# Kernel optimization log

Hardware: AMD Instinct MI355X
Metric: run time of the kernel (lower is better)

Reference implementation:

```python
import jax, jax.numpy as jnp
import numpy as np

N_NODES = 50000
N_EDGES = 800000
D = 128


def sage_conv(x, src, dst, w_nbr, w_root, b, n_nodes):
    # mean aggregation of neighbor features: messages flow src (j) -> dst (i)
    msg_sum = jax.ops.segment_sum(x[src], dst, num_segments=n_nodes)  # [N, D]
    deg = jax.ops.segment_sum(jnp.ones((src.shape[0],), x.dtype), dst,
                              num_segments=n_nodes)
    mean = msg_sum / jnp.maximum(deg, 1.0)[:, None]
    # PyG SAGEConv: lin_l(aggr) + lin_r(x); bias lives in lin_l
    return mean @ w_nbr + x @ w_root + b


def setup_inputs() -> dict:
    key = jax.random.key(0)
    ks = jax.random.split(key, 16)
    s = 1.0 / np.sqrt(D)
    inp = {
        "x": jax.random.normal(ks[0], (N_NODES, D), jnp.float32),
        "edge_index": jax.random.randint(ks[1], (2, N_EDGES), 0, N_NODES,
                                         dtype=jnp.int64),
    }
    for l in range(3):
        inp[f"w_nbr{l}"] = jax.random.normal(ks[2 + 3 * l], (D, D), jnp.float32) * s
        inp[f"w_root{l}"] = jax.random.normal(ks[3 + 3 * l], (D, D), jnp.float32) * s
        inp[f"b{l}"] = jnp.zeros((D,), jnp.float32)
    inp["w_cls"] = jax.random.normal(ks[12], (D, 1), jnp.float32) * s
    inp["b_cls"] = jnp.zeros((1,), jnp.float32)
    return inp


def reference(x, edge_index, w_nbr0, w_root0, b0, w_nbr1, w_root1, b1,
              w_nbr2, w_root2, b2, w_cls, b_cls):
    src, dst = edge_index[0], edge_index[1]
    n = x.shape[0]
    layers = [(w_nbr0, w_root0, b0), (w_nbr1, w_root1, b1), (w_nbr2, w_root2, b2)]
    h = x
    for i, (wn, wr, b) in enumerate(layers):
        h = sage_conv(h, src, dst, wn, wr, b, n)
        if i < len(layers) - 1:
            h = jax.nn.relu(h)  # dropout is identity in eval mode
    return (h @ w_cls + b_cls).squeeze(-1)  # [N]
```

## Files before the change

### kernel.cpp

```cpp
#include <hip/hip_runtime.h>

#define N_NODES 50000
#define N_EDGES 800000
#define D 128
#define NGROUPS 3125
#define NE4 200000
#define NB_E4 782

typedef __attribute__((ext_vector_type(8))) short short8;
typedef __attribute__((ext_vector_type(4))) float f32x4;

__device__ __forceinline__ float bits2f(unsigned int u) {
    union { unsigned int u; float f; } c; c.u = u; return c.f;
}
__device__ __forceinline__ unsigned short f2b(float f) {
    union { float f; unsigned int u; } c; c.f = f;
    unsigned int r = c.u + 0x7fffu + ((c.u >> 16) & 1u);
    return (unsigned short)(r >> 16);
}


__global__ void k_big(const int* __restrict__ dst, int* __restrict__ deg,
                      int* __restrict__ rank, const float* __restrict__ x,
                      const float* __restrict__ wn0, const float* __restrict__ wr0,
                      const float* __restrict__ wn1, const float* __restrict__ wr1,
                      const float* __restrict__ wn2, const float* __restrict__ wr2,
                      const float* __restrict__ b2, const float* __restrict__ wc,
                      const float* __restrict__ bc,
                      unsigned short* __restrict__ f0,
                      unsigned short* __restrict__ f1,
                      unsigned short* __restrict__ f2,
                      unsigned short* __restrict__ Bp,
                      float* __restrict__ uvc) {
    int b = blockIdx.x;
    if (b < NB_E4) {
        int i = b * 256 + threadIdx.x;
        if (i < NE4) {
            int4 d4 = reinterpret_cast<const int4*>(dst)[i];
            int r0 = atomicAdd(&deg[d4.x], 1);
            int r1 = atomicAdd(&deg[d4.y], 1);
            int r2 = atomicAdd(&deg[d4.z], 1);
            int r3 = atomicAdd(&deg[d4.w], 1);
            reinterpret_cast<int4*>(rank)[i] = make_int4(r0, r1, r2, r3);
        }
    } else if (b < 7032) {
        int i = (b - NB_E4) * 256 + threadIdx.x;
        float4 v = reinterpret_cast<const float4*>(x)[i];
        ushort4 o;
        o.x = f2b(v.x); o.y = f2b(v.y); o.z = f2b(v.z); o.w = f2b(v.w);
        reinterpret_cast<ushort4*>(f0)[i] = o;
    } else if (b < 7064) {
        int t = (b - 7032) * 256 + threadIdx.x;
        int layer = t >> 12;
        int rem = t & 4095;
        int kstep = rem >> 9;
        int cf = (rem >> 6) & 7;
        int lane = t & 63;
        const float* W = (kstep < 4) ? (layer ? wn1 : wn0) : (layer ? wr1 : wr0);
        int kb = kstep * 32 + (lane >> 4) * 8;
        int colv = cf * 16 + (lane & 15);
        int koff = (kstep < 4) ? kb : kb - 128;
        unsigned short* dstp = Bp + (((layer * 64 + kstep * 8 + cf) * 64 + lane) << 3);
        #pragma unroll
        for (int i = 0; i < 8; ++i) dstp[i] = f2b(W[(koff + i) * D + colv]);
    } else if (b == 7064) {
        int t = threadIdx.x;
        if (t < D) {
            f0[(size_t)N_NODES * D + t] = 0;
            f1[(size_t)N_NODES * D + t] = 0;
            f2[(size_t)N_NODES * D + t] = 0;
        }
    } else {
        int t = threadIdx.x;
        if (t < 128) {
            float su = 0.f;
            for (int m = 0; m < 128; ++m) su += wn2[t * D + m] * wc[m];
            uvc[t] = su;
        } else {
            int k = t - 128;
            float sv = 0.f;
            for (int m = 0; m < 128; ++m) sv += wr2[k * D + m] * wc[m];
            uvc[128 + k] = sv;
        }
        if (t == 0) {
            float sc = 0.f;
            for (int m = 0; m < 128; ++m) sc += b2[m] * wc[m];
            uvc[256] = sc + bc[0];
        }
    }
}


__global__ void k_scan1(const int* __restrict__ deg, int* __restrict__ rs,
                        int* __restrict__ bsum) {
    __shared__ int wsum[16];
    int tid = threadIdx.x;
    int lane = tid & 63, wid = tid >> 6;
    int i = blockIdx.x * 1024 + tid;
    int v = (i < N_NODES) ? deg[i] : 0;
    int s = v;
    #pragma unroll
    for (int off = 1; off < 64; off <<= 1) {
        int t = __shfl_up(s, off, 64);
        if (lane >= off) s += t;
    }
    if (lane == 63) wsum[wid] = s;
    __syncthreads();
    if (tid < 64) {
        int wv = (tid < 16) ? wsum[tid] : 0;
        int t = wv;
        #pragma unroll
        for (int off = 1; off < 16; off <<= 1) {
            int u = __shfl_up(t, off, 64);
            if (tid >= off) t += u;
        }
        if (tid < 16) wsum[tid] = t - wv;
    }
    __syncthreads();
    int excl = s - v + wsum[wid];
    if (i < N_NODES) rs[i] = excl;
    if (tid == 1023) bsum[blockIdx.x] = excl + v;
}

__global__ void k_scan23(int* __restrict__ rs, const int* __restrict__ bsum,
                         int nb) {
    __shared__ int bp[64];
    if (threadIdx.x < 64) {
        int lane = threadIdx.x;
        int v = (lane < nb) ? bsum[lane] : 0;
        int s = v;
        #pragma unroll
        for (int off = 1; off < 64; off <<= 1) {
            int t = __shfl_up(s, off, 64);
            if (lane >= off) s += t;
        }
        bp[lane] = s - v;
    }
    __syncthreads();
    int i = blockIdx.x * blockDim.x + threadIdx.x;
    if (i < N_NODES) rs[i] += bp[i >> 10];
    if (i == 0) rs[N_NODES] = N_EDGES;
}

__global__ void k_fill2(const int* __restrict__ src, const int* __restrict__ dst,
                        const int* __restrict__ rs, const int* __restrict__ rank,
                        int* __restrict__ col) {
    int i = blockIdx.x * blockDim.x + threadIdx.x;
    if (i >= NE4) return;
    int4 d4 = reinterpret_cast<const int4*>(dst)[i];
    int4 r4 = reinterpret_cast<const int4*>(rank)[i];
    int4 s4 = reinterpret_cast<const int4*>(src)[i];
    int p0 = rs[d4.x], p1 = rs[d4.y], p2 = rs[d4.z], p3 = rs[d4.w];
    col[p0 + r4.x] = s4.x;
    col[p1 + r4.y] = s4.y;
    col[p2 + r4.z] = s4.z;
    col[p3 + r4.w] = s4.w;
}


#define ACCUM(v)                                                      \
    acc0 += bits2f((v).x << 16); acc1 += bits2f((v).x & 0xffff0000u); \
    acc2 += bits2f((v).y << 16); acc3 += bits2f((v).y & 0xffff0000u); \
    acc4 += bits2f((v).z << 16); acc5 += bits2f((v).z & 0xffff0000u); \
    acc6 += bits2f((v).w << 16); acc7 += bits2f((v).w & 0xffff0000u);

__global__ __launch_bounds__(256) void k_agg2(const unsigned short* __restrict__ h,
                                              const int* __restrict__ rs,
                                              const int* __restrict__ col,
                                              unsigned short* __restrict__ mean) {
    const int lane = threadIdx.x & 63;
    const int node = blockIdx.x * 4 + (threadIdx.x >> 6);
    if (node >= N_NODES) return;
    const int j0 = rs[node], j1 = rs[node + 1];
    const int deg = j1 - j0;
    const int q = lane >> 4;
    const int d8 = (lane & 15) * 8;

    int myc = (j0 + lane < j1) ? col[j0 + lane] : N_NODES;
    const int nfull = deg < 64 ? deg : 64;
    const int nb = (nfull + 15) >> 4;

    float acc0 = 0.f, acc1 = 0.f, acc2 = 0.f, acc3 = 0.f;
    float acc4 = 0.f, acc5 = 0.f, acc6 = 0.f, acc7 = 0.f;

    for (int i = 0; i < nb; ++i) {
        int t = (i << 4) + q;
        int c0 = __shfl(myc, t, 64);
        int c1 = __shfl(myc, t + 4, 64);
        int c2 = __shfl(myc, t + 8, 64);
        int c3 = __shfl(myc, t + 12, 64);
        uint4 v0 = *(const uint4*)(h + (size_t)c0 * D + d8);
        uint4 v1 = *(const uint4*)(h + (size_t)c1 * D + d8);
        uint4 v2 = *(const uint4*)(h + (size_t)c2 * D + d8);
        uint4 v3 = *(const uint4*)(h + (size_t)c3 * D + d8);
        ACCUM(v0); ACCUM(v1); ACCUM(v2); ACCUM(v3);
    }
    for (int j = j0 + 64 + q; j < j1; j += 4) {
        int c = col[j];
        uint4 v = *(const uint4*)(h + (size_t)c * D + d8);
        ACCUM(v);
    }

    acc0 += __shfl_xor(acc0, 16, 64); acc0 += __shfl_xor(acc0, 32, 64);
    acc1 += __shfl_xor(acc1, 16, 64); acc1 += __shfl_xor(acc1, 32, 64);
    acc2 += __shfl_xor(acc2, 16, 64); acc2 += __shfl_xor(acc2, 32, 64);
    acc3 += __shfl_xor(acc3, 16, 64); acc3 += __shfl_xor(acc3, 32, 64);
    acc4 += __shfl_xor(acc4, 16, 64); acc4 += __shfl_xor(acc4, 32, 64);
    acc5 += __shfl_xor(acc5, 16, 64); acc5 += __shfl_xor(acc5, 32, 64);
    acc6 += __shfl_xor(acc6, 16, 64); acc6 += __shfl_xor(acc6, 32, 64);
    acc7 += __shfl_xor(acc7, 16, 64); acc7 += __shfl_xor(acc7, 32, 64);

    if (lane < 16) {
        float s = 1.0f / (float)(deg > 0 ? deg : 1);
        uint4 o;
        o.x = (unsigned int)f2b(acc0 * s) | ((unsigned int)f2b(acc1 * s) << 16);
        o.y = (unsigned int)f2b(acc2 * s) | ((unsigned int)f2b(acc3 * s) << 16);
        o.z = (unsigned int)f2b(acc4 * s) | ((unsigned int)f2b(acc5 * s) << 16);
        o.w = (unsigned int)f2b(acc6 * s) | ((unsigned int)f2b(acc7 * s) << 16);
        *reinterpret_cast<uint4*>(mean + (size_t)node * D + d8) = o;
    }
}


__global__ __launch_bounds__(256) void k_gemm(
    const unsigned short* __restrict__ Amean, const unsigned short* __restrict__ Ah,
    const unsigned short* __restrict__ Bp, const float* __restrict__ bias,
    unsigned short* __restrict__ outh) {
    int lane = threadIdx.x & 63;
    int w = blockIdx.x * 4 + (threadIdx.x >> 6);
    int g0 = w * 2;
    if (g0 >= NGROUPS) return;
    int g1ok = (g0 + 1 < NGROUPS);
    int hl = lane & 15;
    int klane = (lane >> 4) * 8;
    int arow0 = g0 * 16 + hl;
    int arow1 = g0 * 16 + 16 + hl;
    if (arow1 > N_NODES) arow1 = N_NODES;

    f32x4 acc0[8], acc1[8];
    #pragma unroll
    for (int i = 0; i < 8; ++i) { acc0[i] = (f32x4)0.0f; acc1[i] = (f32x4)0.0f; }

    const short8* bpv = reinterpret_cast<const short8*>(Bp);
    #pragma unroll
    for (int kstep = 0; kstep < 8; ++kstep) {
        const unsigned short* Asrc = (kstep < 4) ? Amean : Ah;
        int kk = (kstep & 3) * 32 + klane;
        short8 a0 = *reinterpret_cast<const short8*>(Asrc + (size_t)arow0 * D + kk);
        short8 a1 = *reinterpret_cast<const short8*>(Asrc + (size_t)arow1 * D + kk);
        #pragma unroll
        for (int cf = 0; cf < 8; ++cf) {
            short8 b = bpv[(kstep * 8 + cf) * 64 + lane];
            acc0[cf] = __builtin_amdgcn_mfma_f32_16x16x32_bf16(a0, b, acc0[cf], 0, 0, 0);
            acc1[cf] = __builtin_amdgcn_mfma_f32_16x16x32_bf16(a1, b, acc1[cf], 0, 0, 0);
        }
    }

    int rbase0 = g0 * 16 + (lane >> 4) * 4;
    #pragma unroll
    for (int cf = 0; cf < 8; ++cf) {
        int bcol = cf * 16 + hl;
        float bv = bias[bcol];
        #pragma unroll
        for (int i = 0; i < 4; ++i) {
            float v = fmaxf(acc0[cf][i] + bv, 0.f);
            outh[(size_t)(rbase0 + i) * D + bcol] = f2b(v);
            if (g1ok) {
                float v1 = fmaxf(acc1[cf][i] + bv, 0.f);
                outh[(size_t)(rbase0 + 16 + i) * D + bcol] = f2b(v1);
            }
        }
    }
}


__global__ __launch_bounds__(256) void k_gemm_dot(
    const unsigned short* __restrict__ Amean, const unsigned short* __restrict__ Ah,
    const unsigned short* __restrict__ Bp, const float* __restrict__ bias,
    const float* __restrict__ uvc, float* __restrict__ s, float* __restrict__ t) {
    int lane = threadIdx.x & 63;
    int w = blockIdx.x * 4 + (threadIdx.x >> 6);
    int g0 = w * 2;
    if (g0 >= NGROUPS) return;
    int g1ok = (g0 + 1 < NGROUPS);
    int hl = lane & 15;
    int klane = (lane >> 4) * 8;
    int arow0 = g0 * 16 + hl;
    int arow1 = g0 * 16 + 16 + hl;
    if (arow1 > N_NODES) arow1 = N_NODES;

    f32x4 acc0[8], acc1[8];
    #pragma unroll
    for (int i = 0; i < 8; ++i) { acc0[i] = (f32x4)0.0f; acc1[i] = (f32x4)0.0f; }

    const short8* bpv = reinterpret_cast<const short8*>(Bp);
    #pragma unroll
    for (int kstep = 0; kstep < 8; ++kstep) {
        const unsigned short* Asrc = (kstep < 4) ? Amean : Ah;
        int kk = (kstep & 3) * 32 + klane;
        short8 a0 = *reinterpret_cast<const short8*>(Asrc + (size_t)arow0 * D + kk);
        short8 a1 = *reinterpret_cast<const short8*>(Asrc + (size_t)arow1 * D + kk);
        #pragma unroll
        for (int cf = 0; cf < 8; ++cf) {
            short8 b = bpv[(kstep * 8 + cf) * 64 + lane];
            acc0[cf] = __builtin_amdgcn_mfma_f32_16x16x32_bf16(a0, b, acc0[cf], 0, 0, 0);
            acc1[cf] = __builtin_amdgcn_mfma_f32_16x16x32_bf16(a1, b, acc1[cf], 0, 0, 0);
        }
    }

    float ps0[4] = {0.f, 0.f, 0.f, 0.f}, pt0[4] = {0.f, 0.f, 0.f, 0.f};
    float ps1[4] = {0.f, 0.f, 0.f, 0.f}, pt1[4] = {0.f, 0.f, 0.f, 0.f};
    #pragma unroll
    for (int cf = 0; cf < 8; ++cf) {
        int bcol = cf * 16 + hl;
        float bv = bias[bcol];
        float uu = uvc[bcol];
        float vv = uvc[128 + bcol];
        #pragma unroll
        for (int i = 0; i < 4; ++i) {
            float v = fmaxf(acc0[cf][i] + bv, 0.f);
            ps0[i] += v * uu;
            pt0[i] += v * vv;
            float v1 = fmaxf(acc1[cf][i] + bv, 0.f);
            ps1[i] += v1 * uu;
            pt1[i] += v1 * vv;
        }
    }
    #pragma unroll
    for (int m = 1; m < 16; m <<= 1) {
        #pragma unroll
        for (int i = 0; i < 4; ++i) {
            ps0[i] += __shfl_xor(ps0[i], m, 64);
            pt0[i] += __shfl_xor(pt0[i], m, 64);
            ps1[i] += __shfl_xor(ps1[i], m, 64);
            pt1[i] += __shfl_xor(pt1[i], m, 64);
        }
    }
    if (hl == 0) {
        int rbase0 = g0 * 16 + (lane >> 4) * 4;
        #pragma unroll
        for (int i = 0; i < 4; ++i) {
            s[rbase0 + i] = ps0[i];
            t[rbase0 + i] = pt0[i];
            if (g1ok) {
                s[rbase0 + 16 + i] = ps1[i];
                t[rbase0 + 16 + i] = pt1[i];
            }
        }
    }
}

__global__ __launch_bounds__(256) void k_sagg2(const float* __restrict__ s,
                                               const float* __restrict__ t,
                                               const float* __restrict__ uvc,
                                               const int* __restrict__ rs,
                                               const int* __restrict__ col,
                                               float* __restrict__ out) {
    const int lane = threadIdx.x & 63;
    const int hl = lane & 15;
    const int node = blockIdx.x * 16 + (threadIdx.x >> 6) * 4 + (lane >> 4);
    const int j0 = rs[node], j1 = rs[node + 1];
    float sm = 0.f;
    for (int j = j0 + hl; j < j1; j += 16) sm += s[col[j]];
    #pragma unroll
    for (int m = 1; m < 16; m <<= 1) sm += __shfl_xor(sm, m, 64);
    if (hl == 0) {
        int deg = j1 - j0;
        out[node] = sm / (float)(deg > 0 ? deg : 1) + t[node] + uvc[256];
    }
}


extern "C" void kernel_launch(void* const* d_in, const int* in_sizes, int n_in,
                              void* d_out, int out_size, void* d_ws,
                              size_t ws_size, hipStream_t stream) {
    const float* x = (const float*)d_in[0];
    const int* ei = (const int*)d_in[1];
    const int* src = ei;
    const int* dst = ei + N_EDGES;
    const float* wn[3] = {(const float*)d_in[2], (const float*)d_in[5],
                          (const float*)d_in[8]};
    const float* wr[3] = {(const float*)d_in[3], (const float*)d_in[6],
                          (const float*)d_in[9]};
    const float* bs[3] = {(const float*)d_in[4], (const float*)d_in[7],
                          (const float*)d_in[10]};
    const float* wc = (const float*)d_in[11];
    const float* bc = (const float*)d_in[12];
    float* out = (float*)d_out;

    char* ws = (char*)d_ws;
    size_t off = 0;
    auto alloc = [&](size_t bytes) -> void* {
        void* p = (void*)(ws + off);
        off += (bytes + 255) & ~(size_t)255;
        return p;
    };
    const size_t frows = (size_t)(N_NODES + 1) * D;
    int* deg = (int*)alloc(N_NODES * 4);
    int* rs = (int*)alloc((N_NODES + 1) * 4);
    int* rank = (int*)alloc(N_EDGES * 4);
    int* bsum = (int*)alloc(64 * 4);
    int* col = (int*)alloc(N_EDGES * 4);
    unsigned short* f0 = (unsigned short*)alloc(frows * 2);
    unsigned short* f1 = (unsigned short*)alloc(frows * 2);
    unsigned short* f2 = (unsigned short*)alloc(frows * 2);
    unsigned short* Bp = (unsigned short*)alloc(2 * 256 * 128 * 2);
    float* uvc = (float*)alloc(260 * 4);
    float* sbuf = (float*)alloc(N_NODES * 4);
    float* tbuf = (float*)alloc(N_NODES * 4);

    hipMemsetAsync(deg, 0, N_NODES * 4, stream);

    k_big<<<7066, 256, 0, stream>>>(dst, deg, rank, x, wn[0], wr[0], wn[1],
                                    wr[1], wn[2], wr[2], bs[2], wc, bc,
                                    f0, f1, f2, Bp, uvc);

    int nb = (N_NODES + 1023) / 1024;
    k_scan1<<<nb, 1024, 0, stream>>>(deg, rs, bsum);
    k_scan23<<<(N_NODES + 255) / 256, 256, 0, stream>>>(rs, bsum, nb);
    k_fill2<<<NB_E4, 256, 0, stream>>>(src, dst, rs, rank, col);

    const int agg_grid = (N_NODES + 3) / 4;
    const int gemm_grid = ((NGROUPS + 1) / 2 + 3) / 4;
    unsigned short* Bp0 = Bp;
    unsigned short* Bp1 = Bp + 256 * 128;

    k_agg2<<<agg_grid, 256, 0, stream>>>(f0, rs, col, f1);
    k_gemm<<<gemm_grid, 256, 0, stream>>>(f1, f0, Bp0, bs[0], f2);
    k_agg2<<<agg_grid, 256, 0, stream>>>(f2, rs, col, f0);
    k_gemm_dot<<<gemm_grid, 256, 0, stream>>>(f0, f2, Bp1, bs[1], uvc, sbuf,
                                              tbuf);
    k_sagg2<<<NGROUPS, 256, 0, stream>>>(sbuf, tbuf, uvc, rs, col, out);
}
```

Before: 163.1 us.

## Privatize degree counters into eight copies to reduce atomic contention in CSR build

Degree counting now spreads atomics across eight per-block-group copies of the degree array, one edge per thread. The scan kernel combines the copies and writes per-copy prefix offsets back, and the fill kernel adds the offset of the copy each edge used. The aim is less same-address atomic serialization in the histogram. In exchange it adds a larger memset, eight times the degree-array traffic in the scan, an extra gather in fill, and non-vectorized dst loads.

Result: no change. 161.6 us (-0.9%).

```diff
diff --git a/kernel.cpp b/kernel.cpp
--- a/kernel.cpp
+++ b/kernel.cpp
@@ -6,6 +6,7 @@
 #define NGROUPS 3125
 #define NE4 200000
 #define NB_E4 782
+#define NCOPY 8
 
 typedef __attribute__((ext_vector_type(8))) short short8;
 typedef __attribute__((ext_vector_type(4))) float f32x4;
@@ -20,7 +21,7 @@
 }
 
 
-__global__ void k_big(const int* __restrict__ dst, int* __restrict__ deg,
+__global__ void k_big(const int* __restrict__ dst, int* __restrict__ deg8,
                       int* __restrict__ rank, const float* __restrict__ x,
                       const float* __restrict__ wn0, const float* __restrict__ wr0,
                       const float* __restrict__ wn1, const float* __restrict__ wr1,
@@ -33,24 +34,18 @@
                       unsigned short* __restrict__ Bp,
                       float* __restrict__ uvc) {
     int b = blockIdx.x;
-    if (b < NB_E4) {
-        int i = b * 256 + threadIdx.x;
-        if (i < NE4) {
-            int4 d4 = reinterpret_cast<const int4*>(dst)[i];
-            int r0 = atomicAdd(&deg[d4.x], 1);
-            int r1 = atomicAdd(&deg[d4.y], 1);
-            int r2 = atomicAdd(&deg[d4.z], 1);
-            int r3 = atomicAdd(&deg[d4.w], 1);
-            reinterpret_cast<int4*>(rank)[i] = make_int4(r0, r1, r2, r3);
-        }
-    } else if (b < 7032) {
-        int i = (b - NB_E4) * 256 + threadIdx.x;
+    if (b < 3125) {
+        int e = b * 256 + threadIdx.x;
+        int k = b & (NCOPY - 1);
+        rank[e] = atomicAdd(&deg8[k * N_NODES + dst[e]], 1);
+    } else if (b < 9375) {
+        int i = (b - 3125) * 256 + threadIdx.x;
         float4 v = reinterpret_cast<const float4*>(x)[i];
         ushort4 o;
         o.x = f2b(v.x); o.y = f2b(v.y); o.z = f2b(v.z); o.w = f2b(v.w);
         reinterpret_cast<ushort4*>(f0)[i] = o;
-    } else if (b < 7064) {
-        int t = (b - 7032) * 256 + threadIdx.x;
+    } else if (b < 9407) {
+        int t = (b - 9375) * 256 + threadIdx.x;
         int layer = t >> 12;
         int rem = t & 4095;
         int kstep = rem >> 9;
@@ -63,7 +58,7 @@
         unsigned short* dstp = Bp + (((layer * 64 + kstep * 8 + cf) * 64 + lane) << 3);
         #pragma unroll
         for (int i = 0; i < 8; ++i) dstp[i] = f2b(W[(koff + i) * D + colv]);
-    } else if (b == 7064) {
+    } else if (b == 9407) {
         int t = threadIdx.x;
         if (t < D) {
             f0[(size_t)N_NODES * D + t] = 0;
@@ -91,13 +86,23 @@
 }
 
 
-__global__ void k_scan1(const int* __restrict__ deg, int* __restrict__ rs,
+__global__ void k_scan1(int* __restrict__ deg8, int* __restrict__ rs,
                         int* __restrict__ bsum) {
     __shared__ int wsum[16];
     int tid = threadIdx.x;
     int lane = tid & 63, wid = tid >> 6;
     int i = blockIdx.x * 1024 + tid;
-    int v = (i < N_NODES) ? deg[i] : 0;
+    int v = 0;
+    if (i < N_NODES) {
+        int pref[NCOPY];
+        #pragma unroll
+        for (int k = 0; k < NCOPY; ++k) {
+            pref[k] = v;
+            v += deg8[k * N_NODES + i];
+        }
+        #pragma unroll
+        for (int k = 0; k < NCOPY; ++k) deg8[k * N_NODES + i] = pref[k];
+    }
     int s = v;
     #pragma unroll
     for (int off = 1; off < 64; off <<= 1) {
@@ -143,14 +148,19 @@
 }
 
 __global__ void k_fill2(const int* __restrict__ src, const int* __restrict__ dst,
-                        const int* __restrict__ rs, const int* __restrict__ rank,
-                        int* __restrict__ col) {
+                        const int* __restrict__ rs, const int* __restrict__ deg8,
+                        const int* __restrict__ rank, int* __restrict__ col) {
     int i = blockIdx.x * blockDim.x + threadIdx.x;
     if (i >= NE4) return;
+    int k = (i >> 6) & (NCOPY - 1);
+    const int* off8 = deg8 + k * N_NODES;
     int4 d4 = reinterpret_cast<const int4*>(dst)[i];
     int4 r4 = reinterpret_cast<const int4*>(rank)[i];
     int4 s4 = reinterpret_cast<const int4*>(src)[i];
-    int p0 = rs[d4.x], p1 = rs[d4.y], p2 = rs[d4.z], p3 = rs[d4.w];
+    int p0 = rs[d4.x] + off8[d4.x];
+    int p1 = rs[d4.y] + off8[d4.y];
+    int p2 = rs[d4.z] + off8[d4.z];
+    int p3 = rs[d4.w] + off8[d4.w];
     col[p0 + r4.x] = s4.x;
     col[p1 + r4.y] = s4.y;
     col[p2 + r4.z] = s4.z;
@@ -396,7 +406,7 @@
         return p;
     };
     const size_t frows = (size_t)(N_NODES + 1) * D;
-    int* deg = (int*)alloc(N_NODES * 4);
+    int* deg8 = (int*)alloc((size_t)NCOPY * N_NODES * 4);
     int* rs = (int*)alloc((N_NODES + 1) * 4);
     int* rank = (int*)alloc(N_EDGES * 4);
     int* bsum = (int*)alloc(64 * 4);
@@ -409,16 +419,16 @@
     float* sbuf = (float*)alloc(N_NODES * 4);
     float* tbuf = (float*)alloc(N_NODES * 4);
 
-    hipMemsetAsync(deg, 0, N_NODES * 4, stream);
-
-    k_big<<<7066, 256, 0, stream>>>(dst, deg, rank, x, wn[0], wr[0], wn[1],
+    hipMemsetAsync(deg8, 0, (size_t)NCOPY * N_NODES * 4, stream);
+
+    k_big<<<9409, 256, 0, stream>>>(dst, deg8, rank, x, wn[0], wr[0], wn[1],
                                     wr[1], wn[2], wr[2], bs[2], wc, bc,
                                     f0, f1, f2, Bp, uvc);
 
     int nb = (N_NODES + 1023) / 1024;
-    k_scan1<<<nb, 1024, 0, stream>>>(deg, rs, bsum);
+    k_scan1<<<nb, 1024, 0, stream>>>(deg8, rs, bsum);
     k_scan23<<<(N_NODES + 255) / 256, 256, 0, stream>>>(rs, bsum, nb);
-    k_fill2<<<NB_E4, 256, 0, stream>>>(src, dst, rs, rank, col);
+    k_fill2<<<NB_E4, 256, 0, stream>>>(src, dst, rs, deg8, rank, col);
 
     const int agg_grid = (N_NODES + 3) / 4;
     const int gemm_grid = ((NGROUPS + 1) / 2 + 3) / 4;
```

## Build CSR via two-level bucket sort with shared-memory atomics

Applied to the files above, without the earlier changes.

Replaces the global-atomic degree count, rank buffer and three scan/fill kernels with a bucketed counting sort. Each edge block counts edges per 196-node bucket in shared memory, a single scan over the block-by-bucket counts gives offsets, edges are scattered into bucket order, and each bucket block then builds its rows and column indices with shared-memory atomics. This removes contended global atomics and the memset, and makes the scatters more local. In exchange it adds an extra pass over the edges and intermediate edge buffers, and each bucket is handled by a single block.

Result: faster. 140.1 us (-14.1%).

```diff
diff --git a/kernel.cpp b/kernel.cpp
--- a/kernel.cpp
+++ b/kernel.cpp
@@ -4,8 +4,12 @@
 #define N_EDGES 800000
 #define D 128
 #define NGROUPS 3125
-#define NE4 200000
-#define NB_E4 782
+#define NBUK 256
+#define NPB 196
+#define EPB 2048
+#define NBLK 391
+#define LTOT (NBUK * NBLK)
+#define NSCB 98
 
 typedef __attribute__((ext_vector_type(8))) short short8;
 typedef __attribute__((ext_vector_type(4))) float f32x4;
@@ -20,37 +24,38 @@
 }
 
 
-__global__ void k_big(const int* __restrict__ dst, int* __restrict__ deg,
-                      int* __restrict__ rank, const float* __restrict__ x,
-                      const float* __restrict__ wn0, const float* __restrict__ wr0,
-                      const float* __restrict__ wn1, const float* __restrict__ wr1,
-                      const float* __restrict__ wn2, const float* __restrict__ wr2,
-                      const float* __restrict__ b2, const float* __restrict__ wc,
-                      const float* __restrict__ bc,
-                      unsigned short* __restrict__ f0,
-                      unsigned short* __restrict__ f1,
-                      unsigned short* __restrict__ f2,
-                      unsigned short* __restrict__ Bp,
-                      float* __restrict__ uvc) {
+__global__ __launch_bounds__(256) void k_big(
+    const int* __restrict__ dst, int* __restrict__ cnt,
+    const float* __restrict__ x,
+    const float* __restrict__ wn0, const float* __restrict__ wr0,
+    const float* __restrict__ wn1, const float* __restrict__ wr1,
+    const float* __restrict__ wn2, const float* __restrict__ wr2,
+    const float* __restrict__ b2, const float* __restrict__ wc,
+    const float* __restrict__ bc,
+    unsigned short* __restrict__ f0, unsigned short* __restrict__ f1,
+    unsigned short* __restrict__ f2, unsigned short* __restrict__ Bp,
+    float* __restrict__ uvc) {
+    __shared__ int lc[NBUK];
     int b = blockIdx.x;
-    if (b < NB_E4) {
-        int i = b * 256 + threadIdx.x;
-        if (i < NE4) {
-            int4 d4 = reinterpret_cast<const int4*>(dst)[i];
-            int r0 = atomicAdd(&deg[d4.x], 1);
-            int r1 = atomicAdd(&deg[d4.y], 1);
-            int r2 = atomicAdd(&deg[d4.z], 1);
-            int r3 = atomicAdd(&deg[d4.w], 1);
-            reinterpret_cast<int4*>(rank)[i] = make_int4(r0, r1, r2, r3);
-        }
-    } else if (b < 7032) {
-        int i = (b - NB_E4) * 256 + threadIdx.x;
+    int tid = threadIdx.x;
+    if (b < NBLK) {
+        lc[tid] = 0;
+        __syncthreads();
+        #pragma unroll
+        for (int k = 0; k < 8; ++k) {
+            int e = b * EPB + k * 256 + tid;
+            if (e < N_EDGES) atomicAdd(&lc[dst[e] / NPB], 1);
+        }
+        __syncthreads();
+        cnt[b * NBUK + tid] = lc[tid];
+    } else if (b < 6641) {
+        int i = (b - NBLK) * 256 + tid;
         float4 v = reinterpret_cast<const float4*>(x)[i];
         ushort4 o;
         o.x = f2b(v.x); o.y = f2b(v.y); o.z = f2b(v.z); o.w = f2b(v.w);
         reinterpret_cast<ushort4*>(f0)[i] = o;
-    } else if (b < 7064) {
-        int t = (b - 7032) * 256 + threadIdx.x;
+    } else if (b < 6673) {
+        int t = (b - 6641) * 256 + tid;
         int layer = t >> 12;
         int rem = t & 4095;
         int kstep = rem >> 9;
@@ -63,41 +68,44 @@
         unsigned short* dstp = Bp + (((layer * 64 + kstep * 8 + cf) * 64 + lane) << 3);
         #pragma unroll
         for (int i = 0; i < 8; ++i) dstp[i] = f2b(W[(koff + i) * D + colv]);
-    } else if (b == 7064) {
-        int t = threadIdx.x;
-        if (t < D) {
-            f0[(size_t)N_NODES * D + t] = 0;
-            f1[(size_t)N_NODES * D + t] = 0;
-            f2[(size_t)N_NODES * D + t] = 0;
+    } else if (b == 6673) {
+        if (tid < D) {
+            f0[(size_t)N_NODES * D + tid] = 0;
+            f1[(size_t)N_NODES * D + tid] = 0;
+            f2[(size_t)N_NODES * D + tid] = 0;
         }
     } else {
-        int t = threadIdx.x;
-        if (t < 128) {
+        if (tid < 128) {
             float su = 0.f;
-            for (int m = 0; m < 128; ++m) su += wn2[t * D + m] * wc[m];
-            uvc[t] = su;
+            for (int m = 0; m < 128; ++m) su += wn2[tid * D + m] * wc[m];
+            uvc[tid] = su;
         } else {
-            int k = t - 128;
+            int k = tid - 128;
             float sv = 0.f;
             for (int m = 0; m < 128; ++m) sv += wr2[k * D + m] * wc[m];
             uvc[128 + k] = sv;
         }
-        if (t == 0) {
-            float sc = 0.f;
-            for (int m = 0; m < 128; ++m) sc += b2[m] * wc[m];
-            uvc[256] = sc + bc[0];
-        }
-    }
-}
-
-
-__global__ void k_scan1(const int* __restrict__ deg, int* __restrict__ rs,
-                        int* __restrict__ bsum) {
+        if (tid == 0) {
+            float sc0 = 0.f;
+            for (int m = 0; m < 128; ++m) sc0 += b2[m] * wc[m];
+            uvc[256] = sc0 + bc[0];
+        }
+    }
+}
+
+
+__global__ void k_scanA(const int* __restrict__ cnt, int* __restrict__ sc,
+                        int* __restrict__ bsumA) {
     __shared__ int wsum[16];
     int tid = threadIdx.x;
     int lane = tid & 63, wid = tid >> 6;
-    int i = blockIdx.x * 1024 + tid;
-    int v = (i < N_NODES) ? deg[i] : 0;
+    int L = blockIdx.x * 1024 + tid;
+    int v = 0;
+    if (L < LTOT) {
+        int bkt = L / NBLK;
+        int j = L - bkt * NBLK;
+        v = cnt[j * NBUK + bkt];
+    }
     int s = v;
     #pragma unroll
     for (int off = 1; off < 64; off <<= 1) {
@@ -118,43 +126,95 @@
     }
     __syncthreads();
     int excl = s - v + wsum[wid];
-    if (i < N_NODES) rs[i] = excl;
-    if (tid == 1023) bsum[blockIdx.x] = excl + v;
-}
-
-__global__ void k_scan23(int* __restrict__ rs, const int* __restrict__ bsum,
-                         int nb) {
-    __shared__ int bp[64];
-    if (threadIdx.x < 64) {
-        int lane = threadIdx.x;
-        int v = (lane < nb) ? bsum[lane] : 0;
-        int s = v;
-        #pragma unroll
-        for (int off = 1; off < 64; off <<= 1) {
-            int t = __shfl_up(s, off, 64);
-            if (lane >= off) s += t;
-        }
-        bp[lane] = s - v;
-    }
-    __syncthreads();
-    int i = blockIdx.x * blockDim.x + threadIdx.x;
-    if (i < N_NODES) rs[i] += bp[i >> 10];
-    if (i == 0) rs[N_NODES] = N_EDGES;
-}
-
-__global__ void k_fill2(const int* __restrict__ src, const int* __restrict__ dst,
-                        const int* __restrict__ rs, const int* __restrict__ rank,
-                        int* __restrict__ col) {
-    int i = blockIdx.x * blockDim.x + threadIdx.x;
-    if (i >= NE4) return;
-    int4 d4 = reinterpret_cast<const int4*>(dst)[i];
-    int4 r4 = reinterpret_cast<const int4*>(rank)[i];
-    int4 s4 = reinterpret_cast<const int4*>(src)[i];
-    int p0 = rs[d4.x], p1 = rs[d4.y], p2 = rs[d4.z], p3 = rs[d4.w];
-    col[p0 + r4.x] = s4.x;
-    col[p1 + r4.y] = s4.y;
-    col[p2 + r4.z] = s4.z;
-    col[p3 + r4.w] = s4.w;
+    if (L < LTOT) sc[L] = excl;
+    if (tid == 1023) bsumA[blockIdx.x] = excl + v;
+}
+
+
+__global__ __launch_bounds__(256) void k_scatter(
+    const int* __restrict__ src, const int* __restrict__ dst,
+    const int* __restrict__ sc, const int* __restrict__ bsumA,
+    int* __restrict__ ed, int* __restrict__ es) {
+    __shared__ int sb[128];
+    __shared__ int cursor[NBUK];
+    int tid = threadIdx.x, j = blockIdx.x;
+    if (tid < 128) sb[tid] = (tid < NSCB) ? bsumA[tid] : 0;
+    __syncthreads();
+    for (int off = 1; off < 128; off <<= 1) {
+        int t = (tid < 128 && tid >= off) ? sb[tid - off] : 0;
+        __syncthreads();
+        if (tid < 128) sb[tid] += t;
+        __syncthreads();
+    }
+    int L = tid * NBLK + j;
+    int idx = L >> 10;
+    cursor[tid] = sc[L] + (idx ? sb[idx - 1] : 0);
+    __syncthreads();
+    #pragma unroll
+    for (int k = 0; k < 8; ++k) {
+        int e = j * EPB + k * 256 + tid;
+        if (e < N_EDGES) {
+            int d = dst[e];
+            int p = atomicAdd(&cursor[d / NPB], 1);
+            ed[p] = d;
+            es[p] = src[e];
+        }
+    }
+}
+
+
+__global__ __launch_bounds__(256) void k_bucket(
+    const int* __restrict__ sc, const int* __restrict__ bsumA,
+    const int* __restrict__ ed, const int* __restrict__ es,
+    int* __restrict__ rs, int* __restrict__ col) {
+    __shared__ int sb[128];
+    __shared__ int lcnt[NPB];
+    __shared__ int s2[256];
+    __shared__ int cur[NPB];
+    int tid = threadIdx.x, b = blockIdx.x;
+    if (tid < 128) sb[tid] = (tid < NSCB) ? bsumA[tid] : 0;
+    __syncthreads();
+    for (int off = 1; off < 128; off <<= 1) {
+        int t = (tid < 128 && tid >= off) ? sb[tid - off] : 0;
+        __syncthreads();
+        if (tid < 128) sb[tid] += t;
+        __syncthreads();
+    }
+    int L0 = b * NBLK;
+    int i0 = L0 >> 10;
+    int gstart = sc[L0] + (i0 ? sb[i0 - 1] : 0);
+    int bend = N_EDGES;
+    if (b + 1 < NBUK) {
+        int L1 = (b + 1) * NBLK;
+        int i1 = L1 >> 10;
+        bend = sc[L1] + (i1 ? sb[i1 - 1] : 0);
+    }
+    if (tid < NPB) lcnt[tid] = 0;
+    __syncthreads();
+    for (int e = gstart + tid; e < bend; e += 256)
+        atomicAdd(&lcnt[ed[e] - b * NPB], 1);
+    __syncthreads();
+    int v = (tid < NPB) ? lcnt[tid] : 0;
+    s2[tid] = v;
+    __syncthreads();
+    for (int off = 1; off < 256; off <<= 1) {
+        int t = (tid >= off) ? s2[tid - off] : 0;
+        __syncthreads();
+        s2[tid] += t;
+        __syncthreads();
+    }
+    int excl = s2[tid] - v;
+    int node = b * NPB + tid;
+    if (tid < NPB) {
+        if (node <= N_NODES) rs[node] = gstart + excl;
+        cur[tid] = gstart + excl;
+    }
+    __syncthreads();
+    for (int e = gstart + tid; e < bend; e += 256) {
+        int p = atomicAdd(&cur[ed[e] - b * NPB], 1);
+        col[p] = es[e];
+    }
+    if (b == NBUK - 1 && tid == 0) rs[N_NODES] = N_EDGES;
 }
 
 
@@ -396,10 +456,12 @@
         return p;
     };
     const size_t frows = (size_t)(N_NODES + 1) * D;
-    int* deg = (int*)alloc(N_NODES * 4);
+    int* cnt = (int*)alloc((size_t)LTOT * 4);
+    int* sc = (int*)alloc((size_t)LTOT * 4);
+    int* bsumA = (int*)alloc(128 * 4);
+    int* ed = (int*)alloc(N_EDGES * 4);
+    int* es = (int*)alloc(N_EDGES * 4);
     int* rs = (int*)alloc((N_NODES + 1) * 4);
-    int* rank = (int*)alloc(N_EDGES * 4);
-    int* bsum = (int*)alloc(64 * 4);
     int* col = (int*)alloc(N_EDGES * 4);
     unsigned short* f0 = (unsigned short*)alloc(frows * 2);
     unsigned short* f1 = (unsigned short*)alloc(frows * 2);
@@ -409,16 +471,13 @@
     float* sbuf = (float*)alloc(N_NODES * 4);
     float* tbuf = (float*)alloc(N_NODES * 4);
 
-    hipMemsetAsync(deg, 0, N_NODES * 4, stream);
-
-    k_big<<<7066, 256, 0, stream>>>(dst, deg, rank, x, wn[0], wr[0], wn[1],
-                                    wr[1], wn[2], wr[2], bs[2], wc, bc,
+
+    k_big<<<6675, 256, 0, stream>>>(dst, cnt, x, wn[0], wr[0], wn[1], wr[1],
+                                    wn[2], wr[2], bs[2], wc, bc,
                                     f0, f1, f2, Bp, uvc);
-
-    int nb = (N_NODES + 1023) / 1024;
-    k_scan1<<<nb, 1024, 0, stream>>>(deg, rs, bsum);
-    k_scan23<<<(N_NODES + 255) / 256, 256, 0, stream>>>(rs, bsum, nb);
-    k_fill2<<<NB_E4, 256, 0, stream>>>(src, dst, rs, rank, col);
+    k_scanA<<<NSCB, 1024, 0, stream>>>(cnt, sc, bsumA);
+    k_scatter<<<NBLK, 256, 0, stream>>>(src, dst, sc, bsumA, ed, es);
+    k_bucket<<<NBUK, 256, 0, stream>>>(sc, bsumA, ed, es, rs, col);
 
     const int agg_grid = (N_NODES + 3) / 4;
     const int gemm_grid = ((NGROUPS + 1) / 2 + 3) / 4;
```
